# Performance work log

Hardware: AMD Instinct MI355X
Metric: run time of the kernel (lower is better)

Reference implementation:

```python
import jax, jax.numpy as jnp
import numpy as np

N_NODES = 100000
N_EDGES = 1600000
D_FEAT = 64


def setup_inputs() -> dict:
    key = jax.random.key(0)
    k1, k2, k3, k4 = jax.random.split(key, 4)
    inp = jax.random.normal(k1, (N_NODES, D_FEAT), dtype=jnp.float32)
    adj_vals = jax.random.uniform(k2, (N_EDGES,), dtype=jnp.float32)
    adj_rows = jax.random.randint(k3, (N_EDGES,), 0, N_NODES, dtype=jnp.int32)
    adj_cols = jax.random.randint(k4, (N_EDGES,), 0, N_NODES, dtype=jnp.int32)
    return {"input": inp, "adj_vals": adj_vals, "adj_rows": adj_rows, "adj_cols": adj_cols}


def reference(input, adj_vals, adj_rows, adj_cols):
    # SpMM: out = A @ H with A in COO form. out[i] = sum_e vals[e] * H[cols[e]] for rows[e]==i
    msgs = adj_vals[:, None] * jnp.take(input, adj_cols, axis=0)  # [E, D]
    out = jax.ops.segment_sum(msgs, adj_rows, num_segments=N_NODES)  # [N, D]
    return out
```

## Files before the change

### kernel.cpp

```cpp
#include <hip/hip_runtime.h>

#define N_NODES 100000
#define N_EDGES 1600000
#define D_FEAT 64

#define N_PART 8
#define SLICE  (N_EDGES / N_PART)

#define RB_LOG 7
#define ROWS_PER_BUCKET 128
#define N_BUCKET ((N_NODES + ROWS_PER_BUCKET - 1) / ROWS_PER_BUCKET)
#define N_CELL (N_BUCKET * N_PART)

#define COL_BITS 17
#define COL_MASK ((1 << COL_BITS) - 1)

#define CAP 512
#define MAXREC 2048
#define PAD 16
#define OVF_MAX 4096

__global__ __launch_bounds__(256) void scatter_kernel(
    const float* __restrict__ vals, const int* __restrict__ rows,
    const int* __restrict__ cols, int* __restrict__ cursor,
    int2* __restrict__ rec, int4* __restrict__ ovf, int* __restrict__ ovf_cnt)
{
    int part = blockIdx.x & (N_PART - 1);
    int blk  = blockIdx.x >> 3;
    int nblk = gridDim.x >> 3;
    int base = part * SLICE;

    const int4*   rows4 = reinterpret_cast<const int4*>(rows + base);
    const int4*   cols4 = reinterpret_cast<const int4*>(cols + base);
    const float4* vals4 = reinterpret_cast<const float4*>(vals + base);
    const int ngrp = SLICE / 4;

    for (int g = blk * 256 + threadIdx.x; g < ngrp; g += nblk * 256) {
        int4   r4 = rows4[g];
        int4   c4 = cols4[g];
        float4 v4 = vals4[g];

        int r[4] = {r4.x, r4.y, r4.z, r4.w};
        int c[4] = {c4.x, c4.y, c4.z, c4.w};
        float v[4] = {v4.x, v4.y, v4.z, v4.w};

        int pos[4], cell[4];
        #pragma unroll
        for (int j = 0; j < 4; ++j) {
            cell[j] = (r[j] >> RB_LOG) * N_PART + part;
            pos[j]  = atomicAdd(&cursor[cell[j] * PAD], 1);
        }
        #pragma unroll
        for (int j = 0; j < 4; ++j) {
            if (pos[j] < CAP) {
                int packed = ((r[j] & (ROWS_PER_BUCKET - 1)) << COL_BITS) | c[j];
                rec[cell[j] * CAP + pos[j]] = make_int2(packed, __float_as_int(v[j]));
            } else {
                int opos = atomicAdd(ovf_cnt, 1);
                if (opos < OVF_MAX)
                    ovf[opos] = make_int4(r[j], c[j], __float_as_int(v[j]), 0);
            }
        }
    }
}

__global__ __launch_bounds__(256) void gather_kernel(
    const float* __restrict__ H, const int2* __restrict__ rec,
    const int* __restrict__ cursor, const int4* __restrict__ ovf,
    const int* __restrict__ ovf_cnt, float* __restrict__ out)
{
    __shared__ int2           recbuf[MAXREC];
    __shared__ unsigned short order[MAXREC];
    __shared__ int            rstart[ROWS_PER_BUCKET + 1];
    __shared__ int            rcur[ROWS_PER_BUCKET];
    __shared__ int            sbuf[2][ROWS_PER_BUCKET];

    int b = blockIdx.x;
    int tid = threadIdx.x;
    int rg = tid >> 4;
    int fc = tid & 15;
    const float4* H4 = reinterpret_cast<const float4*>(H);

    float4 acc[8];
    #pragma unroll
    for (int k = 0; k < 8; ++k) acc[k] = make_float4(0.f, 0.f, 0.f, 0.f);

    int p = 0;
    int skip = 0;
    while (p < N_PART) {
        if (tid < ROWS_PER_BUCKET) rcur[tid] = 0;
        __syncthreads();

        int n = 0;
        while (n < MAXREC && p < N_PART) {
            int cell = b * N_PART + p;
            int cnt = min(cursor[cell * PAD], CAP) - skip;
            int take = min(cnt, MAXREC - n);
            const int2* src = rec + cell * CAP + skip;
            for (int i = tid; i < take; i += 256) {
                int2 r = src[i];
                recbuf[n + i] = r;
                atomicAdd(&rcur[r.x >> COL_BITS], 1);
            }
            n += take;
            if (take < cnt) { skip += take; break; }
            skip = 0; ++p;
        }
        __syncthreads();

        if (tid < ROWS_PER_BUCKET) sbuf[0][tid] = rcur[tid];
        __syncthreads();
        int src = 0;
        for (int off = 1; off < ROWS_PER_BUCKET; off <<= 1) {
            if (tid < ROWS_PER_BUCKET) {
                int x = sbuf[src][tid];
                if (tid >= off) x += sbuf[src][tid - off];
                sbuf[1 - src][tid] = x;
            }
            __syncthreads();
            src ^= 1;
        }
        if (tid < ROWS_PER_BUCKET) rstart[tid + 1] = sbuf[src][tid];
        if (tid == 0) rstart[0] = 0;
        __syncthreads();
        if (tid < ROWS_PER_BUCKET) rcur[tid] = rstart[tid];
        __syncthreads();

        for (int i = tid; i < n; i += 256) {
            int ro = recbuf[i].x >> COL_BITS;
            int pos = atomicAdd(&rcur[ro], 1);
            order[pos] = (unsigned short)i;
        }
        __syncthreads();

        #pragma unroll
        for (int k = 0; k < 8; ++k) {
            int ro = k * 16 + rg;
            int s = rstart[ro], e2 = rstart[ro + 1];
            int i = s;
            for (; i + 4 <= e2; i += 4) {
                int j0 = order[i], j1 = order[i + 1];
                int j2 = order[i + 2], j3 = order[i + 3];
                int2 r0 = recbuf[j0];
                int2 r1 = recbuf[j1];
                int2 r2 = recbuf[j2];
                int2 r3 = recbuf[j3];
                float4 h0 = H4[(r0.x & COL_MASK) * 16 + fc];
                float4 h1 = H4[(r1.x & COL_MASK) * 16 + fc];
                float4 h2 = H4[(r2.x & COL_MASK) * 16 + fc];
                float4 h3 = H4[(r3.x & COL_MASK) * 16 + fc];
                float v0 = __int_as_float(r0.y);
                float v1 = __int_as_float(r1.y);
                float v2 = __int_as_float(r2.y);
                float v3 = __int_as_float(r3.y);
                acc[k].x += v0 * h0.x; acc[k].y += v0 * h0.y;
                acc[k].z += v0 * h0.z; acc[k].w += v0 * h0.w;
                acc[k].x += v1 * h1.x; acc[k].y += v1 * h1.y;
                acc[k].z += v1 * h1.z; acc[k].w += v1 * h1.w;
                acc[k].x += v2 * h2.x; acc[k].y += v2 * h2.y;
                acc[k].z += v2 * h2.z; acc[k].w += v2 * h2.w;
                acc[k].x += v3 * h3.x; acc[k].y += v3 * h3.y;
                acc[k].z += v3 * h3.z; acc[k].w += v3 * h3.w;
            }
            for (; i < e2; ++i) {
                int j0 = order[i];
                int2 r0 = recbuf[j0];
                float4 h0 = H4[(r0.x & COL_MASK) * 16 + fc];
                float v0 = __int_as_float(r0.y);
                acc[k].x += v0 * h0.x; acc[k].y += v0 * h0.y;
                acc[k].z += v0 * h0.z; acc[k].w += v0 * h0.w;
            }
        }
        __syncthreads();
    }

    int novf = min(*ovf_cnt, OVF_MAX);
    int rowbase = b * ROWS_PER_BUCKET;
    for (int i = 0; i < novf; ++i) {
        int4 o = ovf[i];
        int ro = o.x - rowbase;
        if (ro >= 0 && ro < ROWS_PER_BUCKET && (ro & 15) == rg) {
            float4 h = H4[o.y * 16 + fc];
            float v = __int_as_float(o.z);
            int k = ro >> 4;
            acc[k].x += v * h.x; acc[k].y += v * h.y;
            acc[k].z += v * h.z; acc[k].w += v * h.w;
        }
    }

    #pragma unroll
    for (int k = 0; k < 8; ++k) {
        int row = rowbase + k * 16 + rg;
        if (row < N_NODES)
            reinterpret_cast<float4*>(out)[row * 16 + fc] = acc[k];
    }
}

extern "C" void kernel_launch(void* const* d_in, const int* in_sizes, int n_in,
                              void* d_out, int out_size, void* d_ws, size_t ws_size,
                              hipStream_t stream) {
    const float* H    = (const float*)d_in[0];
    const float* vals = (const float*)d_in[1];
    const int*   rows = (const int*)d_in[2];
    const int*   cols = (const int*)d_in[3];
    float* out = (float*)d_out;

    char* ws = (char*)d_ws;
    int2* rec     = (int2*)ws;
    int*  cursor  = (int*)(rec + N_CELL * CAP);
    int*  ovf_cnt = cursor + N_CELL * PAD;
    int4* ovf     = (int4*)(ovf_cnt + 16);

    hipMemsetAsync(cursor, 0, (N_CELL * PAD + 16) * sizeof(int), stream);

    scatter_kernel<<<2048, 256, 0, stream>>>(vals, rows, cols, cursor, rec, ovf, ovf_cnt);
    gather_kernel<<<N_BUCKET, 256, 0, stream>>>(H, rec, cursor, ovf, ovf_cnt, out);
}
```

Measured before the change: 237.1 us.

## Aggregate scatter atomics via shared histogram and widen gather blocks to 512 threads

The scatter kernel now processes a fixed 2048-edge tile per block, builds a per-bucket histogram in shared memory, and issues one global atomicAdd per non-empty bucket to reserve a contiguous range instead of one global atomic per edge. This cuts global atomic contention, at the cost of a block-wide histogram over all buckets and extra barriers. The gather kernel moves to 512 threads per block with 4 row accumulators per thread instead of 8, and MAXREC is doubled so more records fit per pass. The larger buffer raises shared-memory use per block.

```diff
diff --git a/kernel.cpp b/kernel.cpp
--- a/kernel.cpp
+++ b/kernel.cpp
@@ -16,45 +16,62 @@
 #define COL_MASK ((1 << COL_BITS) - 1)
 
 #define CAP 512
-#define MAXREC 2048
+#define MAXREC 4096
 #define PAD 16
 #define OVF_MAX 4096
+
+#define TILE 2048
+#define EPT (TILE / 256)
+#define SBLK_PER_PART ((SLICE + TILE - 1) / TILE)
 
 __global__ __launch_bounds__(256) void scatter_kernel(
     const float* __restrict__ vals, const int* __restrict__ rows,
     const int* __restrict__ cols, int* __restrict__ cursor,
     int2* __restrict__ rec, int4* __restrict__ ovf, int* __restrict__ ovf_cnt)
 {
+    __shared__ int hcnt[N_BUCKET];
+    __shared__ int hbase[N_BUCKET];
+
     int part = blockIdx.x & (N_PART - 1);
     int blk  = blockIdx.x >> 3;
-    int nblk = gridDim.x >> 3;
     int base = part * SLICE;
-
-    const int4*   rows4 = reinterpret_cast<const int4*>(rows + base);
-    const int4*   cols4 = reinterpret_cast<const int4*>(cols + base);
-    const float4* vals4 = reinterpret_cast<const float4*>(vals + base);
-    const int ngrp = SLICE / 4;
-
-    for (int g = blk * 256 + threadIdx.x; g < ngrp; g += nblk * 256) {
-        int4   r4 = rows4[g];
-        int4   c4 = cols4[g];
-        float4 v4 = vals4[g];
-
-        int r[4] = {r4.x, r4.y, r4.z, r4.w};
-        int c[4] = {c4.x, c4.y, c4.z, c4.w};
-        float v[4] = {v4.x, v4.y, v4.z, v4.w};
-
-        int pos[4], cell[4];
-        #pragma unroll
-        for (int j = 0; j < 4; ++j) {
-            cell[j] = (r[j] >> RB_LOG) * N_PART + part;
-            pos[j]  = atomicAdd(&cursor[cell[j] * PAD], 1);
-        }
-        #pragma unroll
-        for (int j = 0; j < 4; ++j) {
-            if (pos[j] < CAP) {
+    int t0 = blk * TILE;
+
+    for (int i = threadIdx.x; i < N_BUCKET; i += 256) hcnt[i] = 0;
+    __syncthreads();
+
+    int r[EPT], c[EPT], rk[EPT], bb[EPT];
+    float v[EPT];
+    #pragma unroll
+    for (int j = 0; j < EPT; ++j) {
+        int e = t0 + j * 256 + threadIdx.x;
+        if (e < SLICE) {
+            int idx = base + e;
+            r[j] = rows[idx];
+            c[j] = cols[idx];
+            v[j] = vals[idx];
+            bb[j] = r[j] >> RB_LOG;
+            rk[j] = atomicAdd(&hcnt[bb[j]], 1);
+        } else {
+            bb[j] = -1;
+        }
+    }
+    __syncthreads();
+
+    for (int i = threadIdx.x; i < N_BUCKET; i += 256) {
+        int cnt = hcnt[i];
+        if (cnt) hbase[i] = atomicAdd(&cursor[(i * N_PART + part) * PAD], cnt);
+    }
+    __syncthreads();
+
+    #pragma unroll
+    for (int j = 0; j < EPT; ++j) {
+        if (bb[j] >= 0) {
+            int pos = hbase[bb[j]] + rk[j];
+            if (pos < CAP) {
+                int cell = bb[j] * N_PART + part;
                 int packed = ((r[j] & (ROWS_PER_BUCKET - 1)) << COL_BITS) | c[j];
-                rec[cell[j] * CAP + pos[j]] = make_int2(packed, __float_as_int(v[j]));
+                rec[cell * CAP + pos] = make_int2(packed, __float_as_int(v[j]));
             } else {
                 int opos = atomicAdd(ovf_cnt, 1);
                 if (opos < OVF_MAX)
@@ -64,7 +81,7 @@
     }
 }
 
-__global__ __launch_bounds__(256) void gather_kernel(
+__global__ __launch_bounds__(512) void gather_kernel(
     const float* __restrict__ H, const int2* __restrict__ rec,
     const int* __restrict__ cursor, const int4* __restrict__ ovf,
     const int* __restrict__ ovf_cnt, float* __restrict__ out)
@@ -81,9 +98,9 @@
     int fc = tid & 15;
     const float4* H4 = reinterpret_cast<const float4*>(H);
 
-    float4 acc[8];
-    #pragma unroll
-    for (int k = 0; k < 8; ++k) acc[k] = make_float4(0.f, 0.f, 0.f, 0.f);
+    float4 acc[4];
+    #pragma unroll
+    for (int k = 0; k < 4; ++k) acc[k] = make_float4(0.f, 0.f, 0.f, 0.f);
 
     int p = 0;
     int skip = 0;
@@ -97,7 +114,7 @@
             int cnt = min(cursor[cell * PAD], CAP) - skip;
             int take = min(cnt, MAXREC - n);
             const int2* src = rec + cell * CAP + skip;
-            for (int i = tid; i < take; i += 256) {
+            for (int i = tid; i < take; i += 512) {
                 int2 r = src[i];
                 recbuf[n + i] = r;
                 atomicAdd(&rcur[r.x >> COL_BITS], 1);
@@ -126,7 +143,7 @@
         if (tid < ROWS_PER_BUCKET) rcur[tid] = rstart[tid];
         __syncthreads();
 
-        for (int i = tid; i < n; i += 256) {
+        for (int i = tid; i < n; i += 512) {
             int ro = recbuf[i].x >> COL_BITS;
             int pos = atomicAdd(&rcur[ro], 1);
             order[pos] = (unsigned short)i;
@@ -134,8 +151,8 @@
         __syncthreads();
 
         #pragma unroll
-        for (int k = 0; k < 8; ++k) {
-            int ro = k * 16 + rg;
+        for (int k = 0; k < 4; ++k) {
+            int ro = k * 32 + rg;
             int s = rstart[ro], e2 = rstart[ro + 1];
             int i = s;
             for (; i + 4 <= e2; i += 4) {
@@ -179,18 +196,18 @@
     for (int i = 0; i < novf; ++i) {
         int4 o = ovf[i];
         int ro = o.x - rowbase;
-        if (ro >= 0 && ro < ROWS_PER_BUCKET && (ro & 15) == rg) {
+        if (ro >= 0 && ro < ROWS_PER_BUCKET && (ro & 31) == rg) {
             float4 h = H4[o.y * 16 + fc];
             float v = __int_as_float(o.z);
-            int k = ro >> 4;
+            int k = ro >> 5;
             acc[k].x += v * h.x; acc[k].y += v * h.y;
             acc[k].z += v * h.z; acc[k].w += v * h.w;
         }
     }
 
     #pragma unroll
-    for (int k = 0; k < 8; ++k) {
-        int row = rowbase + k * 16 + rg;
+    for (int k = 0; k < 4; ++k) {
+        int row = rowbase + k * 32 + rg;
         if (row < N_NODES)
             reinterpret_cast<float4*>(out)[row * 16 + fc] = acc[k];
     }
@@ -213,6 +230,7 @@
 
     hipMemsetAsync(cursor, 0, (N_CELL * PAD + 16) * sizeof(int), stream);
 
-    scatter_kernel<<<2048, 256, 0, stream>>>(vals, rows, cols, cursor, rec, ovf, ovf_cnt);
-    gather_kernel<<<N_BUCKET, 256, 0, stream>>>(H, rec, cursor, ovf, ovf_cnt, out);
+    scatter_kernel<<<SBLK_PER_PART * N_PART, 256, 0, stream>>>(
+        vals, rows, cols, cursor, rec, ovf, ovf_cnt);
+    gather_kernel<<<N_BUCKET, 512, 0, stream>>>(H, rec, cursor, ovf, ovf_cnt, out);
 }
```

Result: faster. 203.5 us (-14.2%).
